# Optimization experiments

Measured on AMD Instinct MI355X. Metric: run time of the kernel, lower is better.

Reference implementation:

```python
import jax, jax.numpy as jnp
import numpy as np

TEMPERATURE = 0.5
EPS = 1e-10

N, C, H, W = 8, 256, 96, 96
T, V = 32, 256
NUM_CLASSES = 19


def setup_inputs() -> dict:
    key = jax.random.key(0)
    k1, k2, k3, k4 = jax.random.split(key, 4)
    features = jax.random.normal(k1, (N, C, H, W), dtype=jnp.float32)
    batch_inds = jax.random.randint(k2, (T,), 0, N, dtype=jnp.int32)
    sample_inds = jax.random.randint(k3, (T, V), 0, H * W).astype(jnp.int64)
    labels = jax.random.randint(k4, (T,), 0, NUM_CLASSES, dtype=jnp.int32)
    return {"features": features, "batch_inds": batch_inds,
            "sample_inds": sample_inds, "labels": labels}


def reference(features, batch_inds, sample_inds, labels):
    n, c, h, w = features.shape
    t, v = sample_inds.shape
    # --- anchor sampling: gather V pixels per (image, class) pair ---
    f = features.reshape(n, c, h * w)            # (N, C, HW)
    g = f[batch_inds]                            # (T, C, HW)
    sampled = jnp.take_along_axis(g, sample_inds[:, None, :], axis=2)  # (T, C, V)
    # --- contrastive loss ---
    norm = jnp.maximum(jnp.linalg.norm(sampled, axis=1, keepdims=True), 1e-12)
    feats = sampled / norm                       # L2 normalize along C
    feats = jnp.swapaxes(feats, 1, 2).reshape(t * v, c)  # (T*V, C)
    lab = jnp.repeat(labels, v)                  # (T*V,)
    dot = (feats @ feats.T) / TEMPERATURE        # (T*V, T*V)
    eq = (lab[:, None] == lab[None, :]).astype(dot.dtype)
    diag = jnp.eye(t * v, dtype=dot.dtype)
    pos_mask = eq * (1.0 - diag)
    neg_mask = 1.0 - eq
    # stable SupCon loss: logsumexp over {self-exp + all negatives}
    logits = dot - jax.lax.stop_gradient(jnp.max(dot, axis=1, keepdims=True))
    exp_logits = jnp.exp(logits)
    neg_sum = jnp.sum(exp_logits * neg_mask, axis=1, keepdims=True)
    log_prob = logits - jnp.log(exp_logits + neg_sum)
    mean_log_prob_pos = jnp.sum(pos_mask * log_prob, axis=1) / jnp.maximum(
        jnp.sum(pos_mask, axis=1), EPS)
    return -jnp.mean(mean_log_prob_pos)
```

## Files before the change

kernel.cpp:

```cpp
#include <hip/hip_runtime.h>
#include <hip/hip_bf16.h>


namespace {

constexpr int kC = 256;
constexpr int kHW = 96 * 96;
constexpr int kT = 32;
constexpr int kV = 256;
constexpr int kM = kT * kV;

typedef __attribute__((ext_vector_type(8))) short short8;
typedef __attribute__((ext_vector_type(4))) float f32x4;

__device__ inline unsigned short f2bf(float x) {
  __hip_bfloat16 h = __float2bfloat16(x);
  return __builtin_bit_cast(unsigned short, h);
}
__device__ inline float bf2f(unsigned short u) {
  unsigned int v = ((unsigned int)u) << 16;
  return __builtin_bit_cast(float, v);
}
__device__ inline float exp_2am2(float a) {
  return exp2f(fmaf(a, 2.8853900818f, -2.8853900818f));
}

__device__ inline void mfma_agpr(f32x4& acc, const short8& a,
                                 const short8& b) {
  asm("v_mfma_f32_16x16x32_bf16 %0, %1, %2, %0"
      : "+v"(acc)
      : "a"(a), "v"(b));
}


}

__global__ __launch_bounds__(256) void k_prep(
    const int* __restrict__ labels, float* __restrict__ ns,
    float* __restrict__ out, int out_size, int* __restrict__ nact,
    ushort2* __restrict__ list, float* __restrict__ cscale) {
  const int tid = (int)threadIdx.x;
  const int b = (int)blockIdx.x;
  for (int i = b * 256 + tid; i < kM; i += 64 * 256) ns[i] = 0.f;
  if (b != 0) return;
  __shared__ int s_lab[kT];
  if (tid < kT) s_lab[tid] = labels[tid];
  if (tid == 0) *nact = 0;
  for (int i = tid; i < out_size; i += 256) out[i] = 0.f;
  __syncthreads();
  if (tid < kT) {
    int m = 0;
    for (int u = 0; u < kT; ++u) m += (s_lab[u] == s_lab[tid]) ? 1 : 0;
    cscale[tid] = 1.f / ((float)(m * kV - 1) * (float)kM);
  }
  for (int p = tid; p < kT * kT; p += 256) {
    const int ti = p >> 5, tj = p & 31;
    if (s_lab[ti] == s_lab[tj]) {
      int base = atomicAdd(nact, 64);
#pragma unroll
      for (int a = 0; a < 8; ++a)
#pragma unroll
        for (int bb = 0; bb < 8; ++bb) {
          ushort2 e;
          e.x = (unsigned short)(ti * 8 + a);
          e.y = (unsigned short)(tj * 8 + bb);
          list[base + a * 8 + bb] = e;
        }
    }
  }
}

__global__ __launch_bounds__(256) void k_gather(
    const float* __restrict__ feat, const int* __restrict__ binds,
    const int* __restrict__ sinds, unsigned short* __restrict__ FT) {
  const int b = (int)blockIdx.x;
  const int c = (int)blockIdx.y;
  __shared__ alignas(16) float row[kHW];
  __shared__ int s_match[kT + 1];
  if (threadIdx.x == 0) {
    int cnt = 0;
    for (int t = 0; t < kT; ++t)
      if (binds[t] == b) s_match[1 + cnt++] = t;
    s_match[0] = cnt;
  }
  __syncthreads();
  const int cnt = s_match[0];
  if (cnt == 0) return;
  const float4* src4 = (const float4*)(feat + ((size_t)b * kC + c) * kHW);
  for (int i = (int)threadIdx.x; i < kHW / 4; i += 256)
    ((float4*)row)[i] = src4[i];
  __syncthreads();
  unsigned short* dst = FT + (size_t)c * kM;
  for (int mi = 1; mi <= cnt; ++mi) {
    const int t = s_match[mi];
    const int p = sinds[t * kV + threadIdx.x];
    dst[t * kV + threadIdx.x] = f2bf(row[p]);
  }
}

__global__ __launch_bounds__(256) void k_norm(
    const unsigned short* __restrict__ FT, unsigned short* __restrict__ F2) {
  constexpr int PAD = 40;
  const int v0 = (int)blockIdx.x * 32;
  __shared__ alignas(16) unsigned short tile[kC][PAD];
  __shared__ float part[8][32];
  __shared__ float s_inv[32];
  const int tid = (int)threadIdx.x;
  {
    const int p4 = tid & 3, cb = tid >> 2;
    for (int c = cb; c < kC; c += 64) {
      int4 d = *(const int4*)(FT + (size_t)c * kM + v0 + p4 * 8);
      *(int4*)&tile[c][p4 * 8] = d;
    }
  }
  __syncthreads();
  {
    const int v = tid & 31, oct = tid >> 5;
    float ss = 0.f;
    for (int c = oct * 32; c < oct * 32 + 32; ++c) {
      float x = bf2f(tile[c][v]);
      ss += x * x;
    }
    part[oct][v] = ss;
  }
  __syncthreads();
  if (tid < 32) {
    float ss = 0.f;
#pragma unroll
    for (int o = 0; o < 8; ++o) ss += part[o][tid];
    s_inv[tid] = 1.0f / fmaxf(sqrtf(ss), 1e-12f);
  }
  __syncthreads();
#pragma unroll
  for (int p = 0; p < 4; ++p) {
    const int slot = p * 256 + tid;
    const int l16s = slot & 15;
    const int qs = (slot >> 4) & 3;
    const int kss = (slot >> 6) & 7;
    const int gl = slot >> 9;
    const int vloc = gl * 16 + l16s;
    const int c0 = kss * 32 + qs * 8;
    const float inv = s_inv[vloc];
    alignas(16) unsigned short o[8];
#pragma unroll
    for (int k = 0; k < 8; ++k) o[k] = f2bf(bf2f(tile[c0 + k][vloc]) * inv);
    *(int4*)(F2 + ((size_t)(((v0 >> 4) + gl) * 8 + kss) << 9) +
             ((qs * 16 + l16s) << 3)) = *(const int4*)o;
  }
}

__global__ __attribute__((amdgpu_flat_work_group_size(512, 512))) void k_neg(
    const unsigned short* __restrict__ F2, const int* __restrict__ labels,
    float* __restrict__ ns) {
  const int tid = (int)threadIdx.x;
  const int w = tid >> 6, lane = tid & 63, q = lane >> 4, l16 = lane & 15;
  const int bid = (int)blockIdx.x;
  const int panel = bid & 15;
  const int rb = bid >> 4;
  const int rowbase = rb * 512 + w * 64;
  const int labr = labels[rowbase >> 8];
  const bool use0 = (labels[panel * 2] != labr);
  const bool use1 = (labels[panel * 2 + 1] != labr);

  const unsigned short* lanep = F2 + ((q * 16 + l16) << 3);

  short8 af[4][8];
  const int ga = rowbase >> 4;
#pragma unroll
  for (int rg = 0; rg < 4; ++rg)
#pragma unroll
    for (int ks = 0; ks < 8; ++ks)
      af[rg][ks] =
          *(const short8*)(lanep + ((size_t)((ga + rg) * 8 + ks) << 9));

  float sacc[4][4] = {};
  for (int ct = 0; ct < 16; ++ct) {
    const bool use = (ct < 8) ? use0 : use1;
    const int gc = panel * 32 + ct * 2;
    short8 bf[8];
#pragma unroll
    for (int ks = 0; ks < 8; ++ks)
      bf[ks] = *(const short8*)(lanep + ((size_t)(gc * 8 + ks) << 9));
    asm volatile("s_barrier" ::: "memory");
    f32x4 acc0[4];
#pragma unroll
    for (int rg = 0; rg < 4; ++rg) acc0[rg] = (f32x4){0.f, 0.f, 0.f, 0.f};
#pragma unroll
    for (int ks = 0; ks < 8; ++ks)
#pragma unroll
      for (int rg = 0; rg < 4; ++rg) mfma_agpr(acc0[rg], af[rg][ks], bf[ks]);
#pragma unroll
    for (int ks = 0; ks < 8; ++ks)
      bf[ks] =
          *(const short8*)(lanep + ((size_t)((gc + 1) * 8 + ks) << 9));
    f32x4 acc1[4];
#pragma unroll
    for (int rg = 0; rg < 4; ++rg) acc1[rg] = (f32x4){0.f, 0.f, 0.f, 0.f};
#pragma unroll
    for (int ks = 0; ks < 8; ++ks)
#pragma unroll
      for (int rg = 0; rg < 4; ++rg) mfma_agpr(acc1[rg], af[rg][ks], bf[ks]);
    if (use) {
#pragma unroll
      for (int rg = 0; rg < 4; ++rg)
#pragma unroll
        for (int r = 0; r < 4; ++r)
          sacc[rg][r] += exp_2am2(acc0[rg][r]) + exp_2am2(acc1[rg][r]);
    }
  }

#pragma unroll
  for (int rg = 0; rg < 4; ++rg)
#pragma unroll
    for (int r = 0; r < 4; ++r) {
      float v = sacc[rg][r];
      v += __shfl_xor(v, 1, 64);
      v += __shfl_xor(v, 2, 64);
      v += __shfl_xor(v, 4, 64);
      v += __shfl_xor(v, 8, 64);
      if (l16 == 0) atomicAdd(&ns[rowbase + rg * 16 + q * 4 + r], v);
    }
}

__global__ __launch_bounds__(256, 2) void k_pos(
    const unsigned short* __restrict__ F2, const float* __restrict__ ns,
    const int* __restrict__ nact, const ushort2* __restrict__ list,
    const float* __restrict__ cscale, float* __restrict__ out) {
  const int tid = (int)threadIdx.x;
  const int w = tid >> 6, lane = tid & 63, q = lane >> 4, l16 = lane & 15;
  __shared__ float s_pos[4];
  const int n = *nact;
  const unsigned short* lanep = F2 + ((q * 16 + l16) << 3);

  float pos = 0.f;
  for (int idx = (int)blockIdx.x * 4 + w; idx < n;
       idx += (int)gridDim.x * 4) {
    const ushort2 e = list[idx];
    const int r32 = e.x, c32 = e.y;
    const int ga = r32 * 2, gb = c32 * 2;
    short8 af[2][8], bf[2][8];
#pragma unroll
    for (int rg = 0; rg < 2; ++rg)
#pragma unroll
      for (int ks = 0; ks < 8; ++ks) {
        af[rg][ks] =
            *(const short8*)(lanep + ((size_t)((ga + rg) * 8 + ks) << 9));
        bf[rg][ks] =
            *(const short8*)(lanep + ((size_t)((gb + rg) * 8 + ks) << 9));
      }
    float nsv[2][4];
#pragma unroll
    for (int rg = 0; rg < 2; ++rg)
#pragma unroll
      for (int r = 0; r < 4; ++r)
        nsv[rg][r] = ns[r32 * 32 + rg * 16 + q * 4 + r];
    const float scale = cscale[r32 >> 3];

    f32x4 a00 = {0.f, 0.f, 0.f, 0.f}, a01 = a00, a10 = a00, a11 = a00;
#pragma unroll
    for (int ks = 0; ks < 8; ++ks) {
      a00 = __builtin_amdgcn_mfma_f32_16x16x32_bf16(af[0][ks], bf[0][ks], a00,
                                                    0, 0, 0);
      a01 = __builtin_amdgcn_mfma_f32_16x16x32_bf16(af[0][ks], bf[1][ks], a01,
                                                    0, 0, 0);
      a10 = __builtin_amdgcn_mfma_f32_16x16x32_bf16(af[1][ks], bf[0][ks], a10,
                                                    0, 0, 0);
      a11 = __builtin_amdgcn_mfma_f32_16x16x32_bf16(af[1][ks], bf[1][ks], a11,
                                                    0, 0, 0);
    }
    float tpos = 0.f;
#pragma unroll
    for (int rg = 0; rg < 2; ++rg)
#pragma unroll
      for (int cg = 0; cg < 2; ++cg) {
        const f32x4 acc =
            (rg == 0) ? (cg == 0 ? a00 : a01) : (cg == 0 ? a10 : a11);
        const int jc = c32 * 32 + cg * 16 + l16;
#pragma unroll
        for (int r = 0; r < 4; ++r) {
          const int i = r32 * 32 + rg * 16 + q * 4 + r;
          if (i != jc) {
            float d = fmaf(acc[r], 2.f, -2.f);
            tpos += d - __logf(exp_2am2(acc[r]) + nsv[rg][r]);
          }
        }
      }
    pos += scale * tpos;
  }

#pragma unroll
  for (int m = 1; m < 64; m <<= 1) pos += __shfl_xor(pos, m, 64);
  if (lane == 0) s_pos[w] = pos;
  __syncthreads();
  if (tid == 0)
    atomicAdd(out, -(s_pos[0] + s_pos[1] + s_pos[2] + s_pos[3]));
}

extern "C" void kernel_launch(void* const* d_in, const int* in_sizes, int n_in,
                              void* d_out, int out_size, void* d_ws,
                              size_t ws_size, hipStream_t stream) {
  const float* feat = (const float*)d_in[0];
  const int* binds = (const int*)d_in[1];
  const int* sinds = (const int*)d_in[2];
  const int* labels = (const int*)d_in[3];
  float* out = (float*)d_out;
  unsigned short* FT = (unsigned short*)d_ws;
  unsigned short* F2 = FT + (size_t)kC * kM;
  float* ns = (float*)(F2 + (size_t)kM * kC);
  int* nact = (int*)(ns + kM);
  float* cscale = (float*)(nact + 8);
  ushort2* list = (ushort2*)(cscale + 32);

  k_prep<<<64, 256, 0, stream>>>(labels, ns, out, out_size, nact, list, cscale);
  k_gather<<<dim3(8, kC), 256, 0, stream>>>(feat, binds, sinds, FT);
  k_norm<<<kM / 32, 256, 0, stream>>>(FT, F2);
  k_neg<<<256, 512, 0, stream>>>(F2, labels, ns);
  k_pos<<<512, 256, 0, stream>>>(F2, ns, nact, list, cscale, out);
}
```

Baseline: 175.8 us.

## Exploit dot-product symmetry for negatives via pair list with LDS-staged tiles

The negative-sum kernel now walks a list of unordered anchor-block pairs with different labels (ti<tj). For each pair it computes the 256x256 dot tile once and adds the exp sums to both rows and columns, so roughly half of the dense negative work and the work on same-label blocks are skipped. B tiles are double-buffered into LDS through global_load_lds, and A fragments are loaded through LDS. In exchange it adds more LDS atomics, per-job syncthreads, and a grid-stride job loop whose load may be uneven.

```diff
diff --git a/kernel.cpp b/kernel.cpp
--- a/kernel.cpp
+++ b/kernel.cpp
@@ -24,28 +24,49 @@
 __device__ inline float exp_2am2(float a) {
   return exp2f(fmaf(a, 2.8853900818f, -2.8853900818f));
 }
-
-__device__ inline void mfma_agpr(f32x4& acc, const short8& a,
-                                 const short8& b) {
-  asm("v_mfma_f32_16x16x32_bf16 %0, %1, %2, %0"
-      : "+v"(acc)
-      : "a"(a), "v"(b));
-}
-
+__device__ inline void load_lds16(const unsigned short* g, unsigned short* l) {
+  __builtin_amdgcn_global_load_lds(
+      (const __attribute__((address_space(1))) void*)g,
+      (__attribute__((address_space(3))) void*)l, 16, 0, 0);
+}
+
+
+__device__ inline void stage_ct(const unsigned short* __restrict__ F2,
+                                unsigned short* lds, int g0, int tid) {
+#pragma unroll
+  for (int i = 0; i < 2; ++i) {
+    const int nslot = i * 512 + tid;
+    load_lds16(F2 + (((size_t)g0 * 8) << 9) + ((size_t)nslot << 3),
+               lds + ((size_t)nslot << 3));
+  }
+}
+__device__ inline void stage_a(const unsigned short* __restrict__ F2,
+                               unsigned short* lds, int g0, int tid) {
+#pragma unroll
+  for (int i = 0; i < 4; ++i) {
+    const int nslot = i * 512 + tid;
+    load_lds16(F2 + (((size_t)g0 * 8) << 9) + ((size_t)nslot << 3),
+               lds + ((size_t)nslot << 3));
+  }
+}
 
 }
 
 __global__ __launch_bounds__(256) void k_prep(
     const int* __restrict__ labels, float* __restrict__ ns,
     float* __restrict__ out, int out_size, int* __restrict__ nact,
-    ushort2* __restrict__ list, float* __restrict__ cscale) {
+    ushort2* __restrict__ list, float* __restrict__ cscale,
+    int* __restrict__ nneg, ushort2* __restrict__ neglist) {
   const int tid = (int)threadIdx.x;
   const int b = (int)blockIdx.x;
   for (int i = b * 256 + tid; i < kM; i += 64 * 256) ns[i] = 0.f;
   if (b != 0) return;
   __shared__ int s_lab[kT];
   if (tid < kT) s_lab[tid] = labels[tid];
-  if (tid == 0) *nact = 0;
+  if (tid == 0) {
+    *nact = 0;
+    *nneg = 0;
+  }
   for (int i = tid; i < out_size; i += 256) out[i] = 0.f;
   __syncthreads();
   if (tid < kT) {
@@ -66,6 +87,12 @@
           e.y = (unsigned short)(tj * 8 + bb);
           list[base + a * 8 + bb] = e;
         }
+    } else if (ti < tj) {
+      int idx = atomicAdd(nneg, 1);
+      ushort2 e;
+      e.x = (unsigned short)ti;
+      e.y = (unsigned short)tj;
+      neglist[idx] = e;
     }
   }
 }
@@ -149,77 +176,96 @@
   }
 }
 
-__global__ __attribute__((amdgpu_flat_work_group_size(512, 512))) void k_neg(
-    const unsigned short* __restrict__ F2, const int* __restrict__ labels,
-    float* __restrict__ ns) {
+__global__ __launch_bounds__(512, 2) void k_neg(
+    const unsigned short* __restrict__ F2, const int* __restrict__ nneg,
+    const ushort2* __restrict__ neglist, float* __restrict__ ns) {
   const int tid = (int)threadIdx.x;
   const int w = tid >> 6, lane = tid & 63, q = lane >> 4, l16 = lane & 15;
-  const int bid = (int)blockIdx.x;
-  const int panel = bid & 15;
-  const int rb = bid >> 4;
-  const int rowbase = rb * 512 + w * 64;
-  const int labr = labels[rowbase >> 8];
-  const bool use0 = (labels[panel * 2] != labr);
-  const bool use1 = (labels[panel * 2 + 1] != labr);
-
-  const unsigned short* lanep = F2 + ((q * 16 + l16) << 3);
-
-  short8 af[4][8];
-  const int ga = rowbase >> 4;
-#pragma unroll
-  for (int rg = 0; rg < 4; ++rg)
-#pragma unroll
-    for (int ks = 0; ks < 8; ++ks)
-      af[rg][ks] =
-          *(const short8*)(lanep + ((size_t)((ga + rg) * 8 + ks) << 9));
-
-  float sacc[4][4] = {};
-  for (int ct = 0; ct < 16; ++ct) {
-    const bool use = (ct < 8) ? use0 : use1;
-    const int gc = panel * 32 + ct * 2;
-    short8 bf[8];
-#pragma unroll
-    for (int ks = 0; ks < 8; ++ks)
-      bf[ks] = *(const short8*)(lanep + ((size_t)(gc * 8 + ks) << 9));
-    asm volatile("s_barrier" ::: "memory");
-    f32x4 acc0[4];
-#pragma unroll
-    for (int rg = 0; rg < 4; ++rg) acc0[rg] = (f32x4){0.f, 0.f, 0.f, 0.f};
-#pragma unroll
-    for (int ks = 0; ks < 8; ++ks)
-#pragma unroll
-      for (int rg = 0; rg < 4; ++rg) mfma_agpr(acc0[rg], af[rg][ks], bf[ks]);
-#pragma unroll
-    for (int ks = 0; ks < 8; ++ks)
-      bf[ks] =
-          *(const short8*)(lanep + ((size_t)((gc + 1) * 8 + ks) << 9));
-    f32x4 acc1[4];
-#pragma unroll
-    for (int rg = 0; rg < 4; ++rg) acc1[rg] = (f32x4){0.f, 0.f, 0.f, 0.f};
-#pragma unroll
-    for (int ks = 0; ks < 8; ++ks)
-#pragma unroll
-      for (int rg = 0; rg < 4; ++rg) mfma_agpr(acc1[rg], af[rg][ks], bf[ks]);
-    if (use) {
-#pragma unroll
-      for (int rg = 0; rg < 4; ++rg)
-#pragma unroll
-        for (int r = 0; r < 4; ++r)
-          sacc[rg][r] += exp_2am2(acc0[rg][r]) + exp_2am2(acc1[rg][r]);
-    }
-  }
-
-#pragma unroll
-  for (int rg = 0; rg < 4; ++rg)
-#pragma unroll
-    for (int r = 0; r < 4; ++r) {
-      float v = sacc[rg][r];
-      v += __shfl_xor(v, 1, 64);
-      v += __shfl_xor(v, 2, 64);
-      v += __shfl_xor(v, 4, 64);
-      v += __shfl_xor(v, 8, 64);
-      if (l16 == 0) atomicAdd(&ns[rowbase + rg * 16 + q * 4 + r], v);
-    }
+  __shared__ alignas(16) unsigned short Bt[2][8192];
+  __shared__ float colacc[256];
+  const int n = *nneg;
+  const int laneofs = (q * 16 + l16) << 3;
+
+  for (int job = (int)blockIdx.x; job < n; job += (int)gridDim.x) {
+    const ushort2 e = neglist[job];
+    const int ti = e.x, tj = e.y;
+    if (tid < 256) colacc[tid] = 0.f;
+
+    short8 af[2][8];
+#pragma unroll 1
+    for (int p = 0; p < 4; ++p) {
+      stage_a(F2, &Bt[0][0], ti * 16 + p * 4, tid);
+      __syncthreads();
+      if ((w >> 1) == p) {
+        const int lg = (w & 1) * 2;
+#pragma unroll
+        for (int rg = 0; rg < 2; ++rg)
+#pragma unroll
+          for (int ks = 0; ks < 8; ++ks)
+            af[rg][ks] = *(const short8*)(
+                &Bt[0][0] + ((size_t)((lg + rg) * 8 + ks) << 9) + laneofs);
+      }
+      __syncthreads();
+    }
+
+    stage_ct(F2, &Bt[0][0], tj * 16, tid);
+    float rowacc[2][4] = {};
+    int cur = 0;
+#pragma unroll 1
+    for (int ct = 0; ct < 8; ++ct) {
+      __syncthreads();
+      if (ct < 7) stage_ct(F2, &Bt[cur ^ 1][0], tj * 16 + (ct + 1) * 2, tid);
+      const unsigned short* bbase = &Bt[cur][0] + laneofs;
+      f32x4 a00 = {0.f, 0.f, 0.f, 0.f}, a01 = a00, a10 = a00, a11 = a00;
+#pragma unroll
+      for (int ks = 0; ks < 8; ++ks) {
+        short8 b0 = *(const short8*)(bbase + ((size_t)ks << 9));
+        short8 b1 = *(const short8*)(bbase + ((size_t)(8 + ks) << 9));
+        a00 = __builtin_amdgcn_mfma_f32_16x16x32_bf16(af[0][ks], b0, a00,
+                                                      0, 0, 0);
+        a01 = __builtin_amdgcn_mfma_f32_16x16x32_bf16(af[0][ks], b1, a01,
+                                                      0, 0, 0);
+        a10 = __builtin_amdgcn_mfma_f32_16x16x32_bf16(af[1][ks], b0, a10,
+                                                      0, 0, 0);
+        a11 = __builtin_amdgcn_mfma_f32_16x16x32_bf16(af[1][ks], b1, a11,
+                                                      0, 0, 0);
+      }
+      float col0 = 0.f, col1 = 0.f;
+#pragma unroll
+      for (int r = 0; r < 4; ++r) {
+        float e00 = exp_2am2(a00[r]), e01 = exp_2am2(a01[r]);
+        float e10 = exp_2am2(a10[r]), e11 = exp_2am2(a11[r]);
+        rowacc[0][r] += e00 + e01;
+        rowacc[1][r] += e10 + e11;
+        col0 += e00 + e10;
+        col1 += e01 + e11;
+      }
+      col0 += __shfl_xor(col0, 16, 64);
+      col0 += __shfl_xor(col0, 32, 64);
+      col1 += __shfl_xor(col1, 16, 64);
+      col1 += __shfl_xor(col1, 32, 64);
+      if (q == 0) {
+        atomicAdd(&colacc[ct * 32 + l16], col0);
+        atomicAdd(&colacc[ct * 32 + 16 + l16], col1);
+      }
+      cur ^= 1;
+    }
+    __syncthreads();
+    if (tid < 256) atomicAdd(&ns[tj * 256 + tid], colacc[tid]);
+#pragma unroll
+    for (int rg = 0; rg < 2; ++rg)
+#pragma unroll
+      for (int r = 0; r < 4; ++r) {
+        float v = rowacc[rg][r];
+        v += __shfl_xor(v, 1, 64);
+        v += __shfl_xor(v, 2, 64);
+        v += __shfl_xor(v, 4, 64);
+        v += __shfl_xor(v, 8, 64);
+        if (l16 == 0)
+          atomicAdd(&ns[ti * 256 + w * 32 + rg * 16 + q * 4 + r], v);
+      }
+    __syncthreads();
+  }
 }
 
 __global__ __launch_bounds__(256, 2) void k_pos(
@@ -310,10 +356,13 @@
   int* nact = (int*)(ns + kM);
   float* cscale = (float*)(nact + 8);
   ushort2* list = (ushort2*)(cscale + 32);
-
-  k_prep<<<64, 256, 0, stream>>>(labels, ns, out, out_size, nact, list, cscale);
+  int* nneg = (int*)(list + 65536);
+  ushort2* neglist = (ushort2*)(nneg + 8);
+
+  k_prep<<<64, 256, 0, stream>>>(labels, ns, out, out_size, nact, list,
+                                 cscale, nneg, neglist);
   k_gather<<<dim3(8, kC), 256, 0, stream>>>(feat, binds, sinds, FT);
   k_norm<<<kM / 32, 256, 0, stream>>>(FT, F2);
-  k_neg<<<256, 512, 0, stream>>>(F2, labels, ns);
+  k_neg<<<512, 512, 0, stream>>>(F2, nneg, neglist, ns);
   k_pos<<<512, 256, 0, stream>>>(F2, ns, nact, list, cscale, out);
 }
```

Result: faster. 165.3 us (-5.9%).
